# Optimization experiments

Measured on AMD Instinct MI355X. Metric: run time of the kernel, lower is better.

Reference implementation:

```python
import jax, jax.numpy as jnp
import numpy as np

MAX_VARS = 10
EMBED_DIM = 128
PATCH = (16, 16)


def setup_inputs() -> dict:
    key = jax.random.key(0)
    k1, k2, k3, k4 = jax.random.split(key, 4)
    x = jax.random.normal(k1, (16, 8, 512, 512), dtype=jnp.float32)
    in_vars = jax.random.randint(k2, (8,), 0, MAX_VARS, dtype=jnp.int64)
    proj_weights = jax.random.normal(k3, (MAX_VARS, EMBED_DIM, 1, PATCH[0], PATCH[1]), dtype=jnp.float32)
    proj_biases = jax.random.normal(k4, (MAX_VARS, EMBED_DIM), dtype=jnp.float32)
    return {"x": x, "in_vars": in_vars, "proj_weights": proj_weights, "proj_biases": proj_biases}


def reference(x, in_vars, proj_weights, proj_biases):
    # x: [B, V, H, W]; proj_weights: [max_vars, E, 1, ph, pw]
    B, V, H, W = x.shape
    E, ph, pw = proj_weights.shape[1], proj_weights.shape[3], proj_weights.shape[4]
    gh, gw = H // ph, W // pw
    w = proj_weights[in_vars, :, 0]       # [V, E, ph, pw] gathered per-variable weights
    b = proj_biases[in_vars]              # [V, E]
    # kernel==stride grouped conv == non-overlapping patchify + per-variable matmul
    xp = x.reshape(B, V, gh, ph, gw, pw)
    out = jnp.einsum('bvhpwq,vepq->bvhwe', xp, w)  # [B, V, gh, gw, E]
    out = out.reshape(B, V, gh * gw, E) + b[None, :, None, :]
    return out  # [B, V, num_patches, E]
```

## Files before the change

kernel.cpp:

```cpp
#include <hip/hip_runtime.h>

#define NB 16
#define NV 8
#define HW 512
#define PH 16
#define GH 32
#define ED 128
#define KD 256
#define MAXV 10

typedef __bf16 bf16x8 __attribute__((ext_vector_type(8)));
typedef float  f32x4  __attribute__((ext_vector_type(4)));

template<int N> __device__ __forceinline__ void waitvm() {
    __builtin_amdgcn_s_waitcnt(0x0F70 | (N & 0xF) | ((N >> 4) << 14));
}

__global__ __launch_bounds__(256) void pack_weights(const float* __restrict__ w,
                                                    __bf16* __restrict__ packed) {
    int tid = blockIdx.x * 256 + threadIdx.x;
    if (tid >= MAXV * ED * KD) return;
    int t   = tid & 31;
    int n   = (tid >> 5) & 127;
    int kb  = (tid >> 12) & 7;
    int var = tid >> 15;
    int k   = kb * 32 + t;
    float f = w[(var * ED + n) * KD + k];
    packed[tid] = (__bf16)f;
}

__global__ __launch_bounds__(256, 2) void patch_embed(
    const float* __restrict__ x,
    const int*   __restrict__ in_vars,
    const __bf16* __restrict__ wpacked,
    const float* __restrict__ bias,
    float* __restrict__ out)
{
    __shared__ float As[4 * 1024 * 4];

    const int tid  = threadIdx.x;
    const int wv   = tid >> 6;
    const int lane = tid & 63;
    const int lo   = lane & 15;
    const int quad = lane >> 4;
    const int qh   = quad >> 1;
    const int qlo  = quad & 1;

    const int sid = blockIdx.x * 4 + wv;
    const int h   = sid & 31;
    const int v   = (sid >> 5) & 7;
    const int b   = sid >> 8;

    const int var = in_vars[v];

    const char* xstrip = (const char*)(x + (((size_t)(b * NV + v)) * HW + (size_t)h * PH) * HW);
    const __bf16* wbase = wpacked + (size_t)var * (ED * KD);

#define DMA_STAGE(T) { \
        const char* gsrc = xstrip + (T) * 4096 + lane * 16; \
        char* lbase = (char*)As + wv * 16384 + ((T) & 3) * 4096; \
        _Pragma("unroll") for (int c = 0; c < 4; ++c) \
            __builtin_amdgcn_global_load_lds( \
                (const __attribute__((address_space(1))) void*)(gsrc + c * 1024), \
                (__attribute__((address_space(3))) void*)(lbase + c * 1024), 16, 0, 0); }

#define BLOAD(T) { \
        _Pragma("unroll") for (int j = 0; j < 8; ++j) \
            bF[(T) % 3][j] = *(const bf16x8*)&wbase[(T) * 4096 + (j * 16 + lo) * 32 + quad * 8]; }

    bf16x8 bF[3][8];
    f32x4  acc[2][8];
    #pragma unroll
    for (int i = 0; i < 2; ++i)
        #pragma unroll
        for (int j = 0; j < 8; ++j)
            acc[i][j] = (f32x4){0.f, 0.f, 0.f, 0.f};

    DMA_STAGE(0); DMA_STAGE(1); DMA_STAGE(2); DMA_STAGE(3);
    asm volatile("" ::: "memory");
    BLOAD(0); BLOAD(1);
    asm volatile("" ::: "memory");

#define A_ITER(KB, NW) { \
        waitvm<NW>(); \
        asm volatile("" ::: "memory"); \
        const float* st = As + wv * 4096 + ((KB) & 3) * 1024; \
        bf16x8 aF[2]; \
        _Pragma("unroll") for (int i = 0; i < 2; ++i) { \
            int fo = qh * 512 + (i * 16 + lo) * 16 + qlo * 8; \
            f32x4 r0 = *(const f32x4*)&st[fo]; \
            f32x4 r1 = *(const f32x4*)&st[fo + 4]; \
            bf16x8 t; \
            t[0] = (__bf16)r0.x; t[1] = (__bf16)r0.y; t[2] = (__bf16)r0.z; t[3] = (__bf16)r0.w; \
            t[4] = (__bf16)r1.x; t[5] = (__bf16)r1.y; t[6] = (__bf16)r1.z; t[7] = (__bf16)r1.w; \
            aF[i] = t; } \
        _Pragma("unroll") for (int i = 0; i < 2; ++i) \
            _Pragma("unroll") for (int j = 0; j < 8; ++j) \
                acc[i][j] = __builtin_amdgcn_mfma_f32_16x16x32_bf16(aF[i], bF[(KB) % 3][j], acc[i][j], 0, 0, 0); \
        asm volatile("" ::: "memory"); \
        if ((KB) + 2 < 8) BLOAD((KB) + 2); \
        if ((KB) + 4 < 8) DMA_STAGE((KB) + 4); \
        asm volatile("" ::: "memory"); }

    A_ITER(0, 8)
    A_ITER(1, 12)
    A_ITER(2, 16)
    A_ITER(3, 16)
    A_ITER(4, 16)
    A_ITER(5, 12)
    A_ITER(6, 8)
    A_ITER(7, 0)

#undef A_ITER
#undef BLOAD
#undef DMA_STAGE

    float bv_[8];
    #pragma unroll
    for (int j = 0; j < 8; ++j)
        bv_[j] = bias[var * ED + j * 16 + lo];

    const size_t outbase = ((size_t)(b * NV + v)) * (GH * GH) + (size_t)h * GH;
    #pragma unroll
    for (int i = 0; i < 2; ++i) {
        #pragma unroll
        for (int r = 0; r < 4; ++r) {
            int m = i * 16 + quad * 4 + r;
            #pragma unroll
            for (int j = 0; j < 8; ++j) {
                out[(outbase + m) * ED + j * 16 + lo] = acc[i][j][r] + bv_[j];
            }
        }
    }
}

extern "C" void kernel_launch(void* const* d_in, const int* in_sizes, int n_in,
                              void* d_out, int out_size, void* d_ws, size_t ws_size,
                              hipStream_t stream) {
    const float* x       = (const float*)d_in[0];
    const int*   in_vars = (const int*)d_in[1];
    const float* w       = (const float*)d_in[2];
    const float* bias    = (const float*)d_in[3];
    float*       out     = (float*)d_out;
    __bf16*      wpacked = (__bf16*)d_ws;

    hipLaunchKernelGGL(pack_weights, dim3((MAXV * ED * KD + 255) / 256), dim3(256), 0, stream,
                       w, wpacked);
    hipLaunchKernelGGL(patch_embed, dim3(NB * NV * GH / 4), dim3(256), 0, stream,
                       x, in_vars, wpacked, bias, out);
}
```

Baseline: 219.7 us.

## Load activation tiles directly into registers instead of staging through LDS

Replaces the global_load_lds DMA staging of activation patches with direct nontemporal vector loads into a 4-deep register ring, removing LDS use and the manual waitcnt scheduling. Folds the bias into the accumulator initialisation, uses nontemporal stores for the output, and wraps the MFMA block in s_setprio. Register pressure rises a lot (64 floats of prefetched activations plus B fragments and accumulators), which under launch_bounds(256,2) risks spills, and the compiler now decides where the memory waits go.

```diff
diff --git a/kernel.cpp b/kernel.cpp
--- a/kernel.cpp
+++ b/kernel.cpp
@@ -11,10 +11,6 @@
 
 typedef __bf16 bf16x8 __attribute__((ext_vector_type(8)));
 typedef float  f32x4  __attribute__((ext_vector_type(4)));
-
-template<int N> __device__ __forceinline__ void waitvm() {
-    __builtin_amdgcn_s_waitcnt(0x0F70 | (N & 0xF) | ((N >> 4) << 14));
-}
 
 __global__ __launch_bounds__(256) void pack_weights(const float* __restrict__ w,
                                                     __bf16* __restrict__ packed) {
@@ -36,8 +32,6 @@
     const float* __restrict__ bias,
     float* __restrict__ out)
 {
-    __shared__ float As[4 * 1024 * 4];
-
     const int tid  = threadIdx.x;
     const int wv   = tid >> 6;
     const int lane = tid & 63;
@@ -56,69 +50,61 @@
     const char* xstrip = (const char*)(x + (((size_t)(b * NV + v)) * HW + (size_t)h * PH) * HW);
     const __bf16* wbase = wpacked + (size_t)var * (ED * KD);
 
-#define DMA_STAGE(T) { \
-        const char* gsrc = xstrip + (T) * 4096 + lane * 16; \
-        char* lbase = (char*)As + wv * 16384 + ((T) & 3) * 4096; \
-        _Pragma("unroll") for (int c = 0; c < 4; ++c) \
-            __builtin_amdgcn_global_load_lds( \
-                (const __attribute__((address_space(1))) void*)(gsrc + c * 1024), \
-                (__attribute__((address_space(3))) void*)(lbase + c * 1024), 16, 0, 0); }
+    const char* abase = xstrip + qh * 2048 + lo * 64 + qlo * 32;
+
+    f32x4  araw[4][4];
+    bf16x8 bF[2][8];
+    f32x4  acc[2][8];
+
+    #pragma unroll
+    for (int j = 0; j < 8; ++j) {
+        float bv = bias[var * ED + j * 16 + lo];
+        #pragma unroll
+        for (int i = 0; i < 2; ++i)
+            acc[i][j] = (f32x4){bv, bv, bv, bv};
+    }
+
+#define ALOAD(T) { \
+        _Pragma("unroll") for (int i = 0; i < 2; ++i) \
+            _Pragma("unroll") for (int hf = 0; hf < 2; ++hf) \
+                araw[(T) & 3][i * 2 + hf] = __builtin_nontemporal_load( \
+                    (const f32x4*)(abase + (T) * 4096 + i * 1024 + hf * 16)); }
 
 #define BLOAD(T) { \
         _Pragma("unroll") for (int j = 0; j < 8; ++j) \
-            bF[(T) % 3][j] = *(const bf16x8*)&wbase[(T) * 4096 + (j * 16 + lo) * 32 + quad * 8]; }
+            bF[(T) & 1][j] = *(const bf16x8*)&wbase[(T) * 4096 + (j * 16 + lo) * 32 + quad * 8]; }
 
-    bf16x8 bF[3][8];
-    f32x4  acc[2][8];
-    #pragma unroll
-    for (int i = 0; i < 2; ++i)
-        #pragma unroll
-        for (int j = 0; j < 8; ++j)
-            acc[i][j] = (f32x4){0.f, 0.f, 0.f, 0.f};
+    ALOAD(0); BLOAD(0); ALOAD(1); BLOAD(1); ALOAD(2); ALOAD(3);
 
-    DMA_STAGE(0); DMA_STAGE(1); DMA_STAGE(2); DMA_STAGE(3);
-    asm volatile("" ::: "memory");
-    BLOAD(0); BLOAD(1);
-    asm volatile("" ::: "memory");
-
-#define A_ITER(KB, NW) { \
-        waitvm<NW>(); \
-        asm volatile("" ::: "memory"); \
-        const float* st = As + wv * 4096 + ((KB) & 3) * 1024; \
+#define STEP(KB) { \
         bf16x8 aF[2]; \
         _Pragma("unroll") for (int i = 0; i < 2; ++i) { \
-            int fo = qh * 512 + (i * 16 + lo) * 16 + qlo * 8; \
-            f32x4 r0 = *(const f32x4*)&st[fo]; \
-            f32x4 r1 = *(const f32x4*)&st[fo + 4]; \
+            f32x4 r0 = araw[(KB) & 3][i * 2 + 0]; \
+            f32x4 r1 = araw[(KB) & 3][i * 2 + 1]; \
             bf16x8 t; \
             t[0] = (__bf16)r0.x; t[1] = (__bf16)r0.y; t[2] = (__bf16)r0.z; t[3] = (__bf16)r0.w; \
             t[4] = (__bf16)r1.x; t[5] = (__bf16)r1.y; t[6] = (__bf16)r1.z; t[7] = (__bf16)r1.w; \
             aF[i] = t; } \
+        __builtin_amdgcn_s_setprio(1); \
         _Pragma("unroll") for (int i = 0; i < 2; ++i) \
             _Pragma("unroll") for (int j = 0; j < 8; ++j) \
-                acc[i][j] = __builtin_amdgcn_mfma_f32_16x16x32_bf16(aF[i], bF[(KB) % 3][j], acc[i][j], 0, 0, 0); \
-        asm volatile("" ::: "memory"); \
-        if ((KB) + 2 < 8) BLOAD((KB) + 2); \
-        if ((KB) + 4 < 8) DMA_STAGE((KB) + 4); \
-        asm volatile("" ::: "memory"); }
+                acc[i][j] = __builtin_amdgcn_mfma_f32_16x16x32_bf16(aF[i], bF[(KB) & 1][j], acc[i][j], 0, 0, 0); \
+        __builtin_amdgcn_s_setprio(0); \
+        if ((KB) + 4 < 8) ALOAD((KB) + 4); \
+        if ((KB) + 2 < 8) BLOAD((KB) + 2); }
 
-    A_ITER(0, 8)
-    A_ITER(1, 12)
-    A_ITER(2, 16)
-    A_ITER(3, 16)
-    A_ITER(4, 16)
-    A_ITER(5, 12)
-    A_ITER(6, 8)
-    A_ITER(7, 0)
+    STEP(0)
+    STEP(1)
+    STEP(2)
+    STEP(3)
+    STEP(4)
+    STEP(5)
+    STEP(6)
+    STEP(7)
 
-#undef A_ITER
+#undef STEP
 #undef BLOAD
-#undef DMA_STAGE
-
-    float bv_[8];
-    #pragma unroll
-    for (int j = 0; j < 8; ++j)
-        bv_[j] = bias[var * ED + j * 16 + lo];
+#undef ALOAD
 
     const size_t outbase = ((size_t)(b * NV + v)) * (GH * GH) + (size_t)h * GH;
     #pragma unroll
@@ -128,7 +114,8 @@
             int m = i * 16 + quad * 4 + r;
             #pragma unroll
             for (int j = 0; j < 8; ++j) {
-                out[(outbase + m) * ED + j * 16 + lo] = acc[i][j][r] + bv_[j];
+                __builtin_nontemporal_store(acc[i][j][r],
+                    &out[(outbase + m) * ED + j * 16 + lo]);
             }
         }
     }
```

Measured after the change: 223.0 us. Within noise of the previous version (+1.5%).
